# Optimization experiments

Hardware: AMD Instinct MI355X
Metric: run time of the kernel (lower is better)

The kernel has to match this reference:

```python
import jax, jax.numpy as jnp
import numpy as np

N = 8192
IN_F = 512
OUT_F = 256


def setup_inputs() -> dict:
    key = jax.random.key(0)
    k1, k2, k3, k4 = jax.random.split(key, 4)
    return {
        "input": jax.random.normal(k1, (N, IN_F), dtype=jnp.float32),
        "w_s": jax.random.uniform(k2, (N, 1), dtype=jnp.float32),
        "w_r": jax.random.uniform(k3, (N, 1), dtype=jnp.float32),
        "weight": jax.random.normal(k4, (IN_F, OUT_F), dtype=jnp.float32),
    }


def reference(input, w_s, w_r, weight):
    # rank-1 learned adjacency: G = w_s @ w_r^T, symmetrized with abs
    G = w_s @ w_r.T                                  # [N, N]
    aG = jnp.abs(G)
    A = (aG + aG.T) * 0.5                            # symmetric_graph
    # normalise_graph: zero the diagonal (graph - diag(graph)*eye)
    idx = jnp.arange(A.shape[0])
    A = A.at[idx, idx].set(0.0)
    # symmetric degree normalization D^-1/2 A D^-1/2 as row/col scaling
    s = A.sum(axis=1)
    s = jnp.where(s == 0.0, 1.0, s)
    dinv = s ** -0.5                                 # [N]
    normA = dinv[:, None] * A * dinv[None, :]        # == D @ A @ D
    # GCN propagation
    H = input @ weight                               # [N, OUT_F]
    return normA @ H
```

## Files before the change

### kernel.cpp

```cpp
#include <hip/hip_runtime.h>
#include <hip/hip_bf16.h>

#define NR 8192
#define KF 512
#define OF 256

#define WS_AL   0
#define WS_BE   8192
#define WS_GA   16384
#define WS_PU   24576
#define WS_PV   90112
#define WS_U    155648
#define WS_V    155904
#define HB_BYTE_OFF 624640
#define BT_BYTE_OFF (HB_BYTE_OFF + 4194304)

typedef float f32x4 __attribute__((ext_vector_type(4)));
typedef __bf16 bf16x8 __attribute__((ext_vector_type(8)));

__global__ __launch_bounds__(256) void kW(const float* __restrict__ weight,
                                          __hip_bfloat16* __restrict__ BtH) {
    __shared__ float tile[64][65];
    const int t   = blockIdx.x;
    const int k0  = (t & 7) * 64;
    const int c0  = (t >> 3) * 64;
    const int tid = threadIdx.x;
    const int cc  = (tid & 15) * 4;
    const int kr0 = tid >> 4;
#pragma unroll
    for (int it = 0; it < 4; ++it) {
        const int kr = it * 16 + kr0;
        const f32x4 v = *(const f32x4*)(weight + (k0 + kr) * OF + c0 + cc);
        tile[kr][cc + 0] = v[0]; tile[kr][cc + 1] = v[1];
        tile[kr][cc + 2] = v[2]; tile[kr][cc + 3] = v[3];
    }
    __syncthreads();
    __bf16* Bt = (__bf16*)BtH;
    const int cr = tid >> 2;
    const int kq = (tid & 3) * 16;
#pragma unroll
    for (int h = 0; h < 2; ++h) {
        bf16x8 v;
#pragma unroll
        for (int j = 0; j < 8; ++j) v[j] = (__bf16)tile[kq + h * 8 + j][cr];
        *(bf16x8*)(Bt + (c0 + cr) * KF + k0 + kq + h * 8) = v;
    }
}

__global__ __launch_bounds__(512) void k1(const float* __restrict__ input,
                                          const float* __restrict__ w_s,
                                          const float* __restrict__ w_r,
                                          const __hip_bfloat16* __restrict__ BtH,
                                          float* __restrict__ ws,
                                          __hip_bfloat16* __restrict__ HbH) {
    __shared__ float H[32 * 257];
    __shared__ float pl[32], ql[32];
    __shared__ float red[16];

    const int tid  = threadIdx.x;
    const int blk  = blockIdx.x;
    const int base = blk * 32;
    __bf16* Hb = (__bf16*)HbH;
    const __bf16* Bt = (const __bf16*)BtH;

    float la = 0.f, lb = 0.f;
    {
        const int t4 = tid * 4;
#pragma unroll
        for (int i = 0; i < 4; ++i) {
            const f32x4 va = *(const f32x4*)(w_s + i * 2048 + t4);
            const f32x4 vb = *(const f32x4*)(w_r + i * 2048 + t4);
            la += fabsf(va[0]) + fabsf(va[1]) + fabsf(va[2]) + fabsf(va[3]);
            lb += fabsf(vb[0]) + fabsf(vb[1]) + fabsf(vb[2]) + fabsf(vb[3]);
        }
    }
#pragma unroll
    for (int o = 32; o > 0; o >>= 1) {
        la += __shfl_down(la, o);
        lb += __shfl_down(lb, o);
    }
    if ((tid & 63) == 0) { red[tid >> 6] = la; red[8 + (tid >> 6)] = lb; }
    __syncthreads();
    float Sa = 0.f, Sb = 0.f;
#pragma unroll
    for (int i = 0; i < 8; ++i) { Sa += red[i]; Sb += red[8 + i]; }

    if (tid < 32) {
        const int row = base + tid;
        const float a = fabsf(w_s[row]);
        const float b = fabsf(w_r[row]);
        float s = 0.5f * (a * (Sb - b) + b * (Sa - a));
        if (s == 0.f) s = 1.f;
        const float d = 1.0f / sqrtf(s);
        ws[WS_AL + row] = 0.5f * d * a;
        ws[WS_BE + row] = 0.5f * d * b;
        ws[WS_GA + row] = d * d * a * b;
        pl[tid] = d * b;
        ql[tid] = d * a;
    }

    const int w       = tid >> 6;
    const int l       = tid & 63;
    const int rowhalf = w >> 2;
    const int cgrp    = w & 3;
    const int lrow    = l & 15;
    const int khalf   = l >> 4;

    const float*  ap0 = input + (base + rowhalf * 16 + lrow) * KF + khalf * 8;
    const __bf16* bp0 = Bt + (cgrp * 64 + lrow) * KF + khalf * 8;

    f32x4 acc0 = {0.f,0.f,0.f,0.f}, acc1 = {0.f,0.f,0.f,0.f};
    f32x4 acc2 = {0.f,0.f,0.f,0.f}, acc3 = {0.f,0.f,0.f,0.f};
#pragma unroll
    for (int ks = 0; ks < 16; ++ks) {
        const int k0 = ks * 32;
        const f32x4 alo = *(const f32x4*)(ap0 + k0);
        const f32x4 ahi = *(const f32x4*)(ap0 + k0 + 4);
        bf16x8 af;
        af[0]=(__bf16)alo[0]; af[1]=(__bf16)alo[1]; af[2]=(__bf16)alo[2]; af[3]=(__bf16)alo[3];
        af[4]=(__bf16)ahi[0]; af[5]=(__bf16)ahi[1]; af[6]=(__bf16)ahi[2]; af[7]=(__bf16)ahi[3];
        const bf16x8 b0 = *(const bf16x8*)(bp0 + 0 * 16 * KF + k0);
        const bf16x8 b1 = *(const bf16x8*)(bp0 + 1 * 16 * KF + k0);
        const bf16x8 b2 = *(const bf16x8*)(bp0 + 2 * 16 * KF + k0);
        const bf16x8 b3 = *(const bf16x8*)(bp0 + 3 * 16 * KF + k0);
        acc0 = __builtin_amdgcn_mfma_f32_16x16x32_bf16(af, b0, acc0, 0, 0, 0);
        acc1 = __builtin_amdgcn_mfma_f32_16x16x32_bf16(af, b1, acc1, 0, 0, 0);
        acc2 = __builtin_amdgcn_mfma_f32_16x16x32_bf16(af, b2, acc2, 0, 0, 0);
        acc3 = __builtin_amdgcn_mfma_f32_16x16x32_bf16(af, b3, acc3, 0, 0, 0);
    }

    {
        const int hr = rowhalf * 16 + khalf * 4;
        const int hc = cgrp * 64 + lrow;
#pragma unroll
        for (int r = 0; r < 4; ++r) {
            H[(hr + r) * 257 + hc +  0] = acc0[r];
            H[(hr + r) * 257 + hc + 16] = acc1[r];
            H[(hr + r) * 257 + hc + 32] = acc2[r];
            H[(hr + r) * 257 + hc + 48] = acc3[r];
        }
    }
    __syncthreads();

    {
        const int k = tid & 255;
        const float* pv = (tid < 256) ? pl : ql;
        float u = 0.f;
#pragma unroll 8
        for (int r = 0; r < 32; ++r) u += pv[r] * H[r * 257 + k];
        if (tid < 256) ws[WS_PU + blk * 256 + k] = u;
        else           ws[WS_PV + blk * 256 + k] = u;
    }

    {
        const int row = tid & 31;
        const int c0  = (tid >> 5) * 16;
        const float* hp = &H[row * 257 + c0];
        bf16x8 v0, v1;
#pragma unroll
        for (int j = 0; j < 8; ++j) v0[j] = (__bf16)hp[j];
#pragma unroll
        for (int j = 0; j < 8; ++j) v1[j] = (__bf16)hp[8 + j];
        __bf16* dst = Hb + (base + row) * OF + c0;
        *(bf16x8*)dst       = v0;
        *(bf16x8*)(dst + 8) = v1;
    }
}

__global__ __launch_bounds__(256) void k2(float* __restrict__ ws) {
    const int b    = blockIdx.x;
    const bool isV = b >= 8;
    const int kb   = (b & 7) * 32;
    const int t    = threadIdx.x;
    const int k    = kb + (t >> 3);
    const int p0   = t & 7;
    const float* P = ws + (isV ? WS_PV : WS_PU);
    float s = 0.f;
#pragma unroll 8
    for (int j = p0; j < 256; j += 8) s += P[j * 256 + k];
#pragma unroll
    for (int o = 4; o > 0; o >>= 1) s += __shfl_down(s, o, 8);
    if (p0 == 0) ws[(isV ? WS_V : WS_U) + k] = s;
}

__global__ __launch_bounds__(256) void k3(const __hip_bfloat16* __restrict__ HbH,
                                          const float* __restrict__ ws,
                                          float* __restrict__ out) {
    __shared__ float aL[32], bL[32], gL[32], UL[256], VL[256];
    const int tid  = threadIdx.x;
    const int base = blockIdx.x * 32;
    UL[tid] = ws[WS_U + tid];
    VL[tid] = ws[WS_V + tid];
    if (tid < 32) {
        aL[tid] = ws[WS_AL + base + tid];
        bL[tid] = ws[WS_BE + base + tid];
        gL[tid] = ws[WS_GA + base + tid];
    }
    __syncthreads();
    const ushort* Hb = (const ushort*)HbH;
    const int c4 = (tid & 63) * 4;
    const int r0 = (tid >> 6) * 8;
    const float u0 = UL[c4], u1 = UL[c4+1], u2 = UL[c4+2], u3 = UL[c4+3];
    const float v0 = VL[c4], v1 = VL[c4+1], v2 = VL[c4+2], v3 = VL[c4+3];
#pragma unroll
    for (int i = 0; i < 8; ++i) {
        const int r = r0 + i;
        const uint2 hv = *(const uint2*)(Hb + (base + r) * OF + c4);
        const float h0 = __uint_as_float(hv.x << 16);
        const float h1 = __uint_as_float(hv.x & 0xffff0000u);
        const float h2 = __uint_as_float(hv.y << 16);
        const float h3 = __uint_as_float(hv.y & 0xffff0000u);
        const float A = aL[r], B = bL[r], G = gL[r];
        f32x4 o;
        o[0] = A * u0 + B * v0 - G * h0;
        o[1] = A * u1 + B * v1 - G * h1;
        o[2] = A * u2 + B * v2 - G * h2;
        o[3] = A * u3 + B * v3 - G * h3;
        *(f32x4*)(out + (base + r) * OF + c4) = o;
    }
}

extern "C" void kernel_launch(void* const* d_in, const int* in_sizes, int n_in,
                              void* d_out, int out_size, void* d_ws, size_t ws_size,
                              hipStream_t stream) {
    const float* input  = (const float*)d_in[0];
    const float* w_s    = (const float*)d_in[1];
    const float* w_r    = (const float*)d_in[2];
    const float* weight = (const float*)d_in[3];
    float* ws = (float*)d_ws;
    __hip_bfloat16* Hb = (__hip_bfloat16*)((char*)d_ws + HB_BYTE_OFF);
    __hip_bfloat16* Bt = (__hip_bfloat16*)((char*)d_ws + BT_BYTE_OFF);
    float* out = (float*)d_out;

    hipLaunchKernelGGL(kW, dim3(32),  dim3(256), 0, stream, weight, Bt);
    hipLaunchKernelGGL(k1, dim3(256), dim3(512), 0, stream, input, w_s, w_r, Bt, ws, Hb);
    hipLaunchKernelGGL(k2, dim3(16),  dim3(256), 0, stream, ws);
    hipLaunchKernelGGL(k3, dim3(256), dim3(256), 0, stream, Hb, ws, out);
}
```

Measured before the change: 99.60 us.

## Fuse four kernels into two with reassociated reduction and in-kernel flag sync

Replaces the weight-transpose, GEMM, reduction and epilogue kernels with two kernels. The first transposes the weight to bf16 and reduces the input rows weighted by the p/q vectors (reassociating u = p^T(XW) as (p^T X)W). The second finishes the u/v vectors in 16 blocks while every block computes its H tile, then waits on a global atomic flag and writes the output straight from shared memory. This removes the bf16 H round-trip and two launches. It adds a spin-wait that assumes the 16 producer blocks make progress while other blocks are resident, plus a per-element uncoalesced weight transpose.

```diff
diff --git a/kernel.cpp b/kernel.cpp
--- a/kernel.cpp
+++ b/kernel.cpp
@@ -8,84 +8,57 @@
 #define WS_AL   0
 #define WS_BE   8192
 #define WS_GA   16384
-#define WS_PU   24576
-#define WS_PV   90112
-#define WS_U    155648
-#define WS_V    155904
-#define HB_BYTE_OFF 624640
-#define BT_BYTE_OFF (HB_BYTE_OFF + 4194304)
+#define WS_PP   24576
+#define WS_PQ   155648
+#define WS_UP   286720
+#define WS_VP   290816
+#define WS_FLAG 294912
+#define BT_BYTE_OFF 1179904
 
 typedef float f32x4 __attribute__((ext_vector_type(4)));
 typedef __bf16 bf16x8 __attribute__((ext_vector_type(8)));
 
-__global__ __launch_bounds__(256) void kW(const float* __restrict__ weight,
-                                          __hip_bfloat16* __restrict__ BtH) {
-    __shared__ float tile[64][65];
-    const int t   = blockIdx.x;
-    const int k0  = (t & 7) * 64;
-    const int c0  = (t >> 3) * 64;
-    const int tid = threadIdx.x;
-    const int cc  = (tid & 15) * 4;
-    const int kr0 = tid >> 4;
-#pragma unroll
-    for (int it = 0; it < 4; ++it) {
-        const int kr = it * 16 + kr0;
-        const f32x4 v = *(const f32x4*)(weight + (k0 + kr) * OF + c0 + cc);
-        tile[kr][cc + 0] = v[0]; tile[kr][cc + 1] = v[1];
-        tile[kr][cc + 2] = v[2]; tile[kr][cc + 3] = v[3];
-    }
-    __syncthreads();
-    __bf16* Bt = (__bf16*)BtH;
-    const int cr = tid >> 2;
-    const int kq = (tid & 3) * 16;
-#pragma unroll
-    for (int h = 0; h < 2; ++h) {
-        bf16x8 v;
-#pragma unroll
-        for (int j = 0; j < 8; ++j) v[j] = (__bf16)tile[kq + h * 8 + j][cr];
-        *(bf16x8*)(Bt + (c0 + cr) * KF + k0 + kq + h * 8) = v;
-    }
-}
-
-__global__ __launch_bounds__(512) void k1(const float* __restrict__ input,
+__global__ __launch_bounds__(512) void kA(const float* __restrict__ input,
                                           const float* __restrict__ w_s,
                                           const float* __restrict__ w_r,
-                                          const __hip_bfloat16* __restrict__ BtH,
+                                          const float* __restrict__ weight,
                                           float* __restrict__ ws,
-                                          __hip_bfloat16* __restrict__ HbH) {
-    __shared__ float H[32 * 257];
+                                          __hip_bfloat16* __restrict__ BtH) {
+    __shared__ f32x4 red[512];
     __shared__ float pl[32], ql[32];
-    __shared__ float red[16];
-
+    __shared__ float wred[16];
     const int tid  = threadIdx.x;
     const int blk  = blockIdx.x;
     const int base = blk * 32;
-    __bf16* Hb = (__bf16*)HbH;
-    const __bf16* Bt = (const __bf16*)BtH;
+
+    if (blk == 0 && tid == 0) ((unsigned*)ws)[WS_FLAG] = 0u;
+
+    {
+        __bf16* Bt = (__bf16*)BtH;
+        Bt[blk * KF + tid] = (__bf16)weight[tid * OF + blk];
+    }
 
     float la = 0.f, lb = 0.f;
-    {
-        const int t4 = tid * 4;
-#pragma unroll
-        for (int i = 0; i < 4; ++i) {
-            const f32x4 va = *(const f32x4*)(w_s + i * 2048 + t4);
-            const f32x4 vb = *(const f32x4*)(w_r + i * 2048 + t4);
-            la += fabsf(va[0]) + fabsf(va[1]) + fabsf(va[2]) + fabsf(va[3]);
-            lb += fabsf(vb[0]) + fabsf(vb[1]) + fabsf(vb[2]) + fabsf(vb[3]);
-        }
+#pragma unroll
+    for (int i = 0; i < 4; ++i) {
+        const int off = i * 2048 + tid * 4;
+        const f32x4 va = *(const f32x4*)(w_s + off);
+        const f32x4 vb = *(const f32x4*)(w_r + off);
+        la += fabsf(va[0]) + fabsf(va[1]) + fabsf(va[2]) + fabsf(va[3]);
+        lb += fabsf(vb[0]) + fabsf(vb[1]) + fabsf(vb[2]) + fabsf(vb[3]);
     }
 #pragma unroll
     for (int o = 32; o > 0; o >>= 1) {
         la += __shfl_down(la, o);
         lb += __shfl_down(lb, o);
     }
-    if ((tid & 63) == 0) { red[tid >> 6] = la; red[8 + (tid >> 6)] = lb; }
-    __syncthreads();
-    float Sa = 0.f, Sb = 0.f;
-#pragma unroll
-    for (int i = 0; i < 8; ++i) { Sa += red[i]; Sb += red[8 + i]; }
+    if ((tid & 63) == 0) { wred[tid >> 6] = la; wred[8 + (tid >> 6)] = lb; }
+    __syncthreads();
 
     if (tid < 32) {
+        float Sa = 0.f, Sb = 0.f;
+#pragma unroll
+        for (int i = 0; i < 8; ++i) { Sa += wred[i]; Sb += wred[8 + i]; }
         const int row = base + tid;
         const float a = fabsf(w_s[row]);
         const float b = fabsf(w_r[row]);
@@ -98,38 +71,121 @@
         pl[tid] = d * b;
         ql[tid] = d * a;
     }
-
-    const int w       = tid >> 6;
-    const int l       = tid & 63;
-    const int rowhalf = w >> 2;
-    const int cgrp    = w & 3;
-    const int lrow    = l & 15;
-    const int khalf   = l >> 4;
-
-    const float*  ap0 = input + (base + rowhalf * 16 + lrow) * KF + khalf * 8;
-    const __bf16* bp0 = Bt + (cgrp * 64 + lrow) * KF + khalf * 8;
-
-    f32x4 acc0 = {0.f,0.f,0.f,0.f}, acc1 = {0.f,0.f,0.f,0.f};
-    f32x4 acc2 = {0.f,0.f,0.f,0.f}, acc3 = {0.f,0.f,0.f,0.f};
-#pragma unroll
-    for (int ks = 0; ks < 16; ++ks) {
-        const int k0 = ks * 32;
-        const f32x4 alo = *(const f32x4*)(ap0 + k0);
-        const f32x4 ahi = *(const f32x4*)(ap0 + k0 + 4);
-        bf16x8 af;
-        af[0]=(__bf16)alo[0]; af[1]=(__bf16)alo[1]; af[2]=(__bf16)alo[2]; af[3]=(__bf16)alo[3];
-        af[4]=(__bf16)ahi[0]; af[5]=(__bf16)ahi[1]; af[6]=(__bf16)ahi[2]; af[7]=(__bf16)ahi[3];
-        const bf16x8 b0 = *(const bf16x8*)(bp0 + 0 * 16 * KF + k0);
-        const bf16x8 b1 = *(const bf16x8*)(bp0 + 1 * 16 * KF + k0);
-        const bf16x8 b2 = *(const bf16x8*)(bp0 + 2 * 16 * KF + k0);
-        const bf16x8 b3 = *(const bf16x8*)(bp0 + 3 * 16 * KF + k0);
-        acc0 = __builtin_amdgcn_mfma_f32_16x16x32_bf16(af, b0, acc0, 0, 0, 0);
-        acc1 = __builtin_amdgcn_mfma_f32_16x16x32_bf16(af, b1, acc1, 0, 0, 0);
-        acc2 = __builtin_amdgcn_mfma_f32_16x16x32_bf16(af, b2, acc2, 0, 0, 0);
-        acc3 = __builtin_amdgcn_mfma_f32_16x16x32_bf16(af, b3, acc3, 0, 0, 0);
+    __syncthreads();
+
+    const int c4 = (tid & 127) * 4;
+    const int rg = tid >> 7;
+    f32x4 accp = {0.f,0.f,0.f,0.f}, accq = {0.f,0.f,0.f,0.f};
+#pragma unroll
+    for (int r = 0; r < 8; ++r) {
+        const int jl = rg * 8 + r;
+        const f32x4 v = *(const f32x4*)(input + (base + jl) * KF + c4);
+        accp += pl[jl] * v;
+        accq += ql[jl] * v;
+    }
+    red[tid] = accp;
+    __syncthreads();
+    if (tid < 128) {
+        const f32x4 s = red[tid] + red[tid + 128] + red[tid + 256] + red[tid + 384];
+        *(f32x4*)(ws + WS_PP + blk * KF + c4) = s;
+    }
+    __syncthreads();
+    red[tid] = accq;
+    __syncthreads();
+    if (tid < 128) {
+        const f32x4 s = red[tid] + red[tid + 128] + red[tid + 256] + red[tid + 384];
+        *(f32x4*)(ws + WS_PQ + blk * KF + c4) = s;
+    }
+}
+
+__global__ __launch_bounds__(512) void kC(const float* __restrict__ input,
+                                          const __hip_bfloat16* __restrict__ BtH,
+                                          const float* __restrict__ weight,
+                                          float* __restrict__ ws,
+                                          float* __restrict__ out) {
+    __shared__ float H[32 * 257];
+    __shared__ float aL[32], bL[32], gL[32];
+    __shared__ float UL[256], VL[256];
+    __shared__ float r_pl[32], r_ql[32];
+    __shared__ float redp[16][32], redq[16][32];
+    __shared__ float uh[2][256], vh[2][256];
+
+    const int tid  = threadIdx.x;
+    const int blk  = blockIdx.x;
+    const int base = blk * 32;
+    const __bf16* Bt = (const __bf16*)BtH;
+    unsigned* flag = (unsigned*)ws + WS_FLAG;
+
+    if (blk < 16) {
+        const int mloc = tid & 31;
+        const int m    = blk * 32 + mloc;
+        const int bg   = tid >> 5;
+        float sp = 0.f, sq = 0.f;
+        for (int b = bg; b < 256; b += 16) {
+            sp += ws[WS_PP + b * KF + m];
+            sq += ws[WS_PQ + b * KF + m];
+        }
+        redp[bg][mloc] = sp; redq[bg][mloc] = sq;
+        __syncthreads();
+        if (tid < 32) {
+            float tp = 0.f, tq = 0.f;
+#pragma unroll
+            for (int g = 0; g < 16; ++g) { tp += redp[g][tid]; tq += redq[g][tid]; }
+            r_pl[tid] = tp; r_ql[tid] = tq;
+        }
+        __syncthreads();
+        const int k  = tid & 255;
+        const int hf = tid >> 8;
+        float u = 0.f, v = 0.f;
+#pragma unroll
+        for (int mm = 0; mm < 16; ++mm) {
+            const int ml = hf * 16 + mm;
+            const float wv = weight[(blk * 32 + ml) * OF + k];
+            u += r_pl[ml] * wv;
+            v += r_ql[ml] * wv;
+        }
+        uh[hf][k] = u; vh[hf][k] = v;
+        __syncthreads();
+        if (tid < 256) ws[WS_UP + blk * 256 + tid] = uh[0][tid] + uh[1][tid];
+        else {
+            const int k2 = tid - 256;
+            ws[WS_VP + blk * 256 + k2] = vh[0][k2] + vh[1][k2];
+        }
+        __threadfence();
+        __syncthreads();
+        if (tid == 0) atomicAdd(flag, 1u);
     }
 
     {
+        const int w       = tid >> 6;
+        const int l       = tid & 63;
+        const int rowhalf = w >> 2;
+        const int cgrp    = w & 3;
+        const int lrow    = l & 15;
+        const int khalf   = l >> 4;
+
+        const float*  ap0 = input + (base + rowhalf * 16 + lrow) * KF + khalf * 8;
+        const __bf16* bp0 = Bt + (cgrp * 64 + lrow) * KF + khalf * 8;
+
+        f32x4 acc0 = {0.f,0.f,0.f,0.f}, acc1 = {0.f,0.f,0.f,0.f};
+        f32x4 acc2 = {0.f,0.f,0.f,0.f}, acc3 = {0.f,0.f,0.f,0.f};
+#pragma unroll
+        for (int ks = 0; ks < 16; ++ks) {
+            const int k0 = ks * 32;
+            const f32x4 alo = *(const f32x4*)(ap0 + k0);
+            const f32x4 ahi = *(const f32x4*)(ap0 + k0 + 4);
+            bf16x8 af;
+            af[0]=(__bf16)alo[0]; af[1]=(__bf16)alo[1]; af[2]=(__bf16)alo[2]; af[3]=(__bf16)alo[3];
+            af[4]=(__bf16)ahi[0]; af[5]=(__bf16)ahi[1]; af[6]=(__bf16)ahi[2]; af[7]=(__bf16)ahi[3];
+            const bf16x8 b0 = *(const bf16x8*)(bp0 + 0 * 16 * KF + k0);
+            const bf16x8 b1 = *(const bf16x8*)(bp0 + 1 * 16 * KF + k0);
+            const bf16x8 b2 = *(const bf16x8*)(bp0 + 2 * 16 * KF + k0);
+            const bf16x8 b3 = *(const bf16x8*)(bp0 + 3 * 16 * KF + k0);
+            acc0 = __builtin_amdgcn_mfma_f32_16x16x32_bf16(af, b0, acc0, 0, 0, 0);
+            acc1 = __builtin_amdgcn_mfma_f32_16x16x32_bf16(af, b1, acc1, 0, 0, 0);
+            acc2 = __builtin_amdgcn_mfma_f32_16x16x32_bf16(af, b2, acc2, 0, 0, 0);
+            acc3 = __builtin_amdgcn_mfma_f32_16x16x32_bf16(af, b3, acc3, 0, 0, 0);
+        }
         const int hr = rowhalf * 16 + khalf * 4;
         const int hc = cgrp * 64 + lrow;
 #pragma unroll
@@ -140,83 +196,47 @@
             H[(hr + r) * 257 + hc + 48] = acc3[r];
         }
     }
-    __syncthreads();
-
-    {
-        const int k = tid & 255;
-        const float* pv = (tid < 256) ? pl : ql;
-        float u = 0.f;
-#pragma unroll 8
-        for (int r = 0; r < 32; ++r) u += pv[r] * H[r * 257 + k];
-        if (tid < 256) ws[WS_PU + blk * 256 + k] = u;
-        else           ws[WS_PV + blk * 256 + k] = u;
-    }
-
-    {
-        const int row = tid & 31;
-        const int c0  = (tid >> 5) * 16;
-        const float* hp = &H[row * 257 + c0];
-        bf16x8 v0, v1;
-#pragma unroll
-        for (int j = 0; j < 8; ++j) v0[j] = (__bf16)hp[j];
-#pragma unroll
-        for (int j = 0; j < 8; ++j) v1[j] = (__bf16)hp[8 + j];
-        __bf16* dst = Hb + (base + row) * OF + c0;
-        *(bf16x8*)dst       = v0;
-        *(bf16x8*)(dst + 8) = v1;
-    }
-}
-
-__global__ __launch_bounds__(256) void k2(float* __restrict__ ws) {
-    const int b    = blockIdx.x;
-    const bool isV = b >= 8;
-    const int kb   = (b & 7) * 32;
-    const int t    = threadIdx.x;
-    const int k    = kb + (t >> 3);
-    const int p0   = t & 7;
-    const float* P = ws + (isV ? WS_PV : WS_PU);
-    float s = 0.f;
-#pragma unroll 8
-    for (int j = p0; j < 256; j += 8) s += P[j * 256 + k];
-#pragma unroll
-    for (int o = 4; o > 0; o >>= 1) s += __shfl_down(s, o, 8);
-    if (p0 == 0) ws[(isV ? WS_V : WS_U) + k] = s;
-}
-
-__global__ __launch_bounds__(256) void k3(const __hip_bfloat16* __restrict__ HbH,
-                                          const float* __restrict__ ws,
-                                          float* __restrict__ out) {
-    __shared__ float aL[32], bL[32], gL[32], UL[256], VL[256];
-    const int tid  = threadIdx.x;
-    const int base = blockIdx.x * 32;
-    UL[tid] = ws[WS_U + tid];
-    VL[tid] = ws[WS_V + tid];
     if (tid < 32) {
         aL[tid] = ws[WS_AL + base + tid];
         bL[tid] = ws[WS_BE + base + tid];
         gL[tid] = ws[WS_GA + base + tid];
     }
     __syncthreads();
-    const ushort* Hb = (const ushort*)HbH;
-    const int c4 = (tid & 63) * 4;
-    const int r0 = (tid >> 6) * 8;
-    const float u0 = UL[c4], u1 = UL[c4+1], u2 = UL[c4+2], u3 = UL[c4+3];
-    const float v0 = VL[c4], v1 = VL[c4+1], v2 = VL[c4+2], v3 = VL[c4+3];
-#pragma unroll
-    for (int i = 0; i < 8; ++i) {
-        const int r = r0 + i;
-        const uint2 hv = *(const uint2*)(Hb + (base + r) * OF + c4);
-        const float h0 = __uint_as_float(hv.x << 16);
-        const float h1 = __uint_as_float(hv.x & 0xffff0000u);
-        const float h2 = __uint_as_float(hv.y << 16);
-        const float h3 = __uint_as_float(hv.y & 0xffff0000u);
-        const float A = aL[r], B = bL[r], G = gL[r];
-        f32x4 o;
-        o[0] = A * u0 + B * v0 - G * h0;
-        o[1] = A * u1 + B * v1 - G * h1;
-        o[2] = A * u2 + B * v2 - G * h2;
-        o[3] = A * u3 + B * v3 - G * h3;
-        *(f32x4*)(out + (base + r) * OF + c4) = o;
+
+    if (tid == 0) {
+        while (__hip_atomic_load(flag, __ATOMIC_ACQUIRE, __HIP_MEMORY_SCOPE_AGENT) < 16u)
+            __builtin_amdgcn_s_sleep(8);
+    }
+    __syncthreads();
+    if (tid < 256) {
+        float s = 0.f;
+#pragma unroll
+        for (int g = 0; g < 16; ++g) s += ws[WS_UP + g * 256 + tid];
+        UL[tid] = s;
+    } else {
+        const int k2 = tid - 256;
+        float s = 0.f;
+#pragma unroll
+        for (int g = 0; g < 16; ++g) s += ws[WS_VP + g * 256 + k2];
+        VL[k2] = s;
+    }
+    __syncthreads();
+
+    {
+        const int c0 = (tid & 63) * 4;
+        const int r0 = (tid >> 6) * 4;
+#pragma unroll
+        for (int i = 0; i < 4; ++i) {
+            const int row = r0 + i;
+            const float A = aL[row], B = bL[row], G = gL[row];
+            const float* hp = &H[row * 257 + c0];
+            f32x4 o;
+            o[0] = A * UL[c0 + 0] + B * VL[c0 + 0] - G * hp[0];
+            o[1] = A * UL[c0 + 1] + B * VL[c0 + 1] - G * hp[1];
+            o[2] = A * UL[c0 + 2] + B * VL[c0 + 2] - G * hp[2];
+            o[3] = A * UL[c0 + 3] + B * VL[c0 + 3] - G * hp[3];
+            *(f32x4*)(out + (base + row) * OF + c0) = o;
+        }
     }
 }
 
@@ -228,12 +248,9 @@
     const float* w_r    = (const float*)d_in[2];
     const float* weight = (const float*)d_in[3];
     float* ws = (float*)d_ws;
-    __hip_bfloat16* Hb = (__hip_bfloat16*)((char*)d_ws + HB_BYTE_OFF);
     __hip_bfloat16* Bt = (__hip_bfloat16*)((char*)d_ws + BT_BYTE_OFF);
     float* out = (float*)d_out;
 
-    hipLaunchKernelGGL(kW, dim3(32),  dim3(256), 0, stream, weight, Bt);
-    hipLaunchKernelGGL(k1, dim3(256), dim3(512), 0, stream, input, w_s, w_r, Bt, ws, Hb);
-    hipLaunchKernelGGL(k2, dim3(16),  dim3(256), 0, stream, ws);
-    hipLaunchKernelGGL(k3, dim3(256), dim3(256), 0, stream, Hb, ws, out);
+    hipLaunchKernelGGL(kA, dim3(256), dim3(512), 0, stream, input, w_s, w_r, weight, ws, Bt);
+    hipLaunchKernelGGL(kC, dim3(256), dim3(512), 0, stream, input, Bt, weight, ws, out);
 }
```

Measured after the change: 107.7 us. 8.1% more time.
